# Performance work log

Measured on AMD Instinct MI355X. Metric: run time of the kernel, lower is better.

The kernel has to match this reference:

```python
import jax, jax.numpy as jnp
import numpy as np

N_HEAD = 16

def setup_inputs() -> dict:
    key = jax.random.key(0)
    k1, k2, k3 = jax.random.split(key, 3)
    B, T, C = 4, 2048, 1024
    x = jax.random.normal(k1, (B, T, C), dtype=jnp.float32)
    w_attn = jax.random.normal(k2, (C, 3 * C), dtype=jnp.float32) * 0.02
    w_o = jax.random.normal(k3, (C, C), dtype=jnp.float32) * 0.02
    return {"x": x, "w_attn": w_attn, "w_o": w_o}

def reference(x, w_attn, w_o):
    B, T, C = x.shape
    H = N_HEAD
    hs = C // H
    qkv = x @ w_attn  # [B,T,3C]
    q, k, v = jnp.split(qkv, 3, axis=-1)
    # [B,H,T,hs]
    q = q.reshape(B, T, H, hs).transpose(0, 2, 1, 3)
    k = k.reshape(B, T, H, hs).transpose(0, 2, 1, 3)
    v = v.reshape(B, T, H, hs).transpose(0, 2, 1, 3)
    att = jnp.einsum('bhqd,bhkd->bhqk', q, k) * (1.0 / np.sqrt(hs).astype(np.float32))
    causal = jnp.tril(jnp.ones((T, T), dtype=bool))
    att = jnp.where(causal[None, None], att, jnp.float32(-jnp.inf))
    att = jax.nn.softmax(att, axis=-1)
    y = jnp.einsum('bhqk,bhkd->bhqd', att, v)
    y = y.transpose(0, 2, 1, 3).reshape(B, T, C)
    return y @ w_o
```

## Files before the change

kernel.cpp:

```cpp
#include <hip/hip_runtime.h>

typedef unsigned short u16;
typedef unsigned int u32;
typedef __attribute__((ext_vector_type(8))) __bf16 bf16x8;
typedef __attribute__((ext_vector_type(4))) float f32x4;
typedef __attribute__((ext_vector_type(8))) unsigned short u16x8;
typedef __attribute__((ext_vector_type(4))) unsigned int u32x4;

typedef const __attribute__((address_space(1))) u32 gu32;
typedef __attribute__((address_space(3))) u32 lu32;

__device__ __forceinline__ u16 f2b(float f) {
  u32 u = __builtin_bit_cast(u32, f);
  u32 r = u + 0x7fffu + ((u >> 16) & 1u);
  return (u16)(r >> 16);
}

__device__ __forceinline__ u32 pk2(float lo, float hi) {
  u32 d;
  asm("v_cvt_pk_bf16_f32 %0, %1, %2" : "=v"(d) : "v"(lo), "v"(hi));
  return d;
}

__device__ __forceinline__ bf16x8 pack8(f32x4 a, f32x4 b) {
  u32x4 u;
  u[0] = pk2(a[0], a[1]);
  u[1] = pk2(a[2], a[3]);
  u[2] = pk2(b[0], b[1]);
  u[3] = pk2(b[2], b[3]);
  return __builtin_bit_cast(bf16x8, u);
}

__device__ __forceinline__ bf16x8 ld8(const u16* p) {
  return __builtin_bit_cast(bf16x8, *(const u16x8*)p);
}

__device__ __forceinline__ void gll16(const void* g, void* l) {
  __builtin_amdgcn_global_load_lds((gu32*)g, (lu32*)l, 16, 0, 0);
}

__device__ __forceinline__ f32x4 mfma16(bf16x8 a, bf16x8 b, f32x4 c) {
  return __builtin_amdgcn_mfma_f32_16x16x32_bf16(a, b, c, 0, 0, 0);
}

__global__ void k_cvt(const float* __restrict__ in, u16* __restrict__ out, int n4) {
  int i = blockIdx.x * blockDim.x + threadIdx.x;
  int stride = gridDim.x * blockDim.x;
  for (int idx = i; idx < n4; idx += stride) {
    float4 v = ((const float4*)in)[idx];
    u32 lo = (u32)f2b(v.x) | ((u32)f2b(v.y) << 16);
    u32 hi = (u32)f2b(v.z) | ((u32)f2b(v.w) << 16);
    ((uint2*)out)[idx] = make_uint2(lo, hi);
  }
}

__global__ void k_tr(const float* __restrict__ in, u16* __restrict__ out, int R, int C) {
  __shared__ u16 tile[32][33];
  int bx = blockIdx.x * 32;
  int by = blockIdx.y * 32;
  int tx = threadIdx.x, ty = threadIdx.y;
#pragma unroll
  for (int i = 0; i < 32; i += 8)
    tile[ty + i][tx] = f2b(in[(size_t)(by + ty + i) * C + bx + tx]);
  __syncthreads();
#pragma unroll
  for (int i = 0; i < 32; i += 8)
    out[(size_t)(bx + ty + i) * R + by + tx] = tile[tx][ty + i];
}

template <int EPI>
__global__ __launch_bounds__(256) void k_gemm(const u16* __restrict__ A,
                                              const u16* __restrict__ B,
                                              void* __restrict__ Cp) {
  const int K = 1024;
  __shared__ __align__(16) u16 As[128 * 32];
  __shared__ __align__(16) u16 Bs[128 * 32];
  int tid = threadIdx.x;
  int lane = tid & 63, wid = tid >> 6;
  int wr = wid >> 1, wc = wid & 1;
  int m0 = blockIdx.y * 128, n0 = blockIdx.x * 128;
  int r = lane & 15, qq = lane >> 4;

  const u16* Ag0 = A + (size_t)(m0 + wid * 32 + (lane >> 2)) * K + (lane & 3) * 8;
  const u16* Bg0 = B + (size_t)(n0 + wid * 32 + (lane >> 2)) * K + (lane & 3) * 8;
  u16* Asl0 = As + (wid * 32) * 32;
  u16* Asl1 = As + (wid * 32 + 16) * 32;
  u16* Bsl0 = Bs + (wid * 32) * 32;
  u16* Bsl1 = Bs + (wid * 32 + 16) * 32;

  f32x4 acc[4][4] = {};

  for (int k0 = 0; k0 < K; k0 += 32) {
    gll16(Ag0 + k0, Asl0);
    gll16(Ag0 + 16 * K + k0, Asl1);
    gll16(Bg0 + k0, Bsl0);
    gll16(Bg0 + 16 * K + k0, Bsl1);
    __syncthreads();
    bf16x8 af[4], bfr[4];
#pragma unroll
    for (int m = 0; m < 4; ++m) af[m] = ld8(&As[(wr * 64 + m * 16 + r) * 32 + qq * 8]);
#pragma unroll
    for (int n = 0; n < 4; ++n) bfr[n] = ld8(&Bs[(wc * 64 + n * 16 + r) * 32 + qq * 8]);
#pragma unroll
    for (int m = 0; m < 4; ++m)
#pragma unroll
      for (int n = 0; n < 4; ++n) acc[m][n] = mfma16(af[m], bfr[n], acc[m][n]);
    __syncthreads();
  }

  if constexpr (EPI == 0) {
    u16* qkv = (u16*)Cp;
#pragma unroll
    for (int m = 0; m < 4; ++m) {
      int gr = m0 + wr * 64 + m * 16 + qq * 4;
      int b = gr >> 11, t0 = gr & 2047;
#pragma unroll
      for (int n = 0; n < 4; ++n) {
        int gc = n0 + wc * 64 + n * 16 + r;
        int which = gc >> 10, rem = gc & 1023;
        int hh = rem >> 6, d = rem & 63;
        if (which == 2) {
          u16* dst = qkv + (size_t)2 * 8388608u +
                     ((size_t)((b * 16 + hh) * 64 + d)) * 2048 + t0;
          u32 p0 = pk2(acc[m][n][0], acc[m][n][1]);
          u32 p1 = pk2(acc[m][n][2], acc[m][n][3]);
          *(uint2*)dst = make_uint2(p0, p1);
        } else {
          float sc = (which == 0) ? 0.18033688011112042f : 1.0f;
          u16* dst = qkv + (size_t)which * 8388608u +
                     ((size_t)((b * 16 + hh) * 2048 + t0)) * 64 + d;
#pragma unroll
          for (int i = 0; i < 4; ++i) dst[(size_t)i * 64] = f2b(acc[m][n][i] * sc);
        }
      }
    }
  } else {
    float* out = (float*)Cp;
#pragma unroll
    for (int m = 0; m < 4; ++m) {
      int gr = m0 + wr * 64 + m * 16 + qq * 4;
#pragma unroll
      for (int n = 0; n < 4; ++n) {
        int gc = n0 + wc * 64 + n * 16 + r;
#pragma unroll
        for (int i = 0; i < 4; ++i) out[(size_t)(gr + i) * 1024 + gc] = acc[m][n][i];
      }
    }
  }
}

__global__ __launch_bounds__(256) void k_attn(const u16* __restrict__ Qm,
                                              const u16* __restrict__ Km,
                                              const u16* __restrict__ VTm,
                                              u16* __restrict__ Y) {
  int bi = blockIdx.x;
  int x = bi >> 6;
  int bh = bi & 63;
  int b = bh >> 4, h = bh & 15;
  int qb0 = (15 - x) * 128;
  int tid = threadIdx.x, lane = tid & 63, w = tid >> 6;
  int r = lane & 15, qq = lane >> 4;
  const size_t base = (size_t)bh * (2048 * 64);
  int q0w = qb0 + w * 32;

  __shared__ __align__(16) u16 Kt[2][64 * 64];
  __shared__ __align__(16) u16 Vt[2][64 * 64];

  bf16x8 qf[2][2];
#pragma unroll
  for (int m = 0; m < 2; ++m)
#pragma unroll
    for (int kc = 0; kc < 2; ++kc)
      qf[m][kc] = ld8(Qm + base + (size_t)(q0w + m * 16 + r) * 64 + kc * 32 + qq * 8);

  f32x4 acc[2][4] = {};
  float m_run[2] = {-1e30f, -1e30f};
  float l_run[2] = {0.f, 0.f};
  int ntwg = (qb0 >> 6) + 2;

  int srow = lane >> 3;
  int kch0 = (lane & 7) ^ (srow & 3);
  int kch1 = (lane & 7) ^ ((srow & 3) | 4);
  int vch = (lane & 7) ^ srow;
  const u16* Kg = Km + base;
  const u16* Vg = VTm + base;

  int ar = 8 * (r >> 2) + (r & 3);
  int fkl = (r & 3) | (((r >> 2) & 1) << 2);
  int ks0 = ((qq ^ fkl)) * 8, ks1 = ((qq ^ fkl) ^ 4) * 8;
  int fvl = r & 7;
  int vs0 = ((qq ^ fvl)) * 8, vs1 = ((qq ^ fvl) ^ 4) * 8;

#define STAGE(buf, j0n)                                                                 \
  do {                                                                                  \
    gll16(Kg + (size_t)((j0n) + w * 16 + srow) * 64 + kch0 * 8,                         \
          &Kt[buf][(w * 16) * 64]);                                                     \
    gll16(Kg + (size_t)((j0n) + w * 16 + 8 + srow) * 64 + kch1 * 8,                     \
          &Kt[buf][(w * 16 + 8) * 64]);                                                 \
    gll16(Vg + (size_t)(w * 16 + srow) * 2048 + (j0n) + vch * 8,                        \
          &Vt[buf][(w * 16) * 64]);                                                     \
    gll16(Vg + (size_t)(w * 16 + 8 + srow) * 2048 + (j0n) + vch * 8,                    \
          &Vt[buf][(w * 16 + 8) * 64]);                                                 \
  } while (0)

  STAGE(0, 0);
  __syncthreads();

  for (int it = 0; it < ntwg; ++it) {
    int j0 = it << 6;
    int cur = it & 1;
    bool active = (j0 <= q0w + 31);
    f32x4 s[4][2];
    bf16x8 vfr[4][2];

    if (active) {
      __builtin_amdgcn_s_setprio(1);
#pragma unroll
      for (int nt = 0; nt < 4; ++nt) {
        int knt = 32 * (nt >> 1) + 4 * (nt & 1);
        const u16* kb_ = &Kt[cur][(knt + ar) * 64];
        bf16x8 k0 = ld8(kb_ + ks0);
        bf16x8 k1 = ld8(kb_ + ks1);
#pragma unroll
        for (int m = 0; m < 2; ++m) {
          f32x4 z = {};
          s[nt][m] = mfma16(k1, qf[m][1], mfma16(k0, qf[m][0], z));
        }
      }
#pragma unroll
      for (int n = 0; n < 4; ++n) {
        const u16* vb_ = &Vt[cur][(n * 16 + r) * 64];
        vfr[n][0] = ld8(vb_ + vs0);
        vfr[n][1] = ld8(vb_ + vs1);
      }
      __builtin_amdgcn_s_setprio(0);
    }

    if (it + 1 < ntwg) STAGE(cur ^ 1, j0 + 64);

    if (active) {
      bool nm = (j0 + 63 > q0w);
      if (nm) {
#pragma unroll
        for (int nt = 0; nt < 4; ++nt) {
          int kb = j0 + 32 * (nt >> 1) + 4 * (nt & 1) + 8 * qq;
#pragma unroll
          for (int m = 0; m < 2; ++m) {
            int qg = q0w + m * 16 + r;
#pragma unroll
            for (int i = 0; i < 4; ++i)
              s[nt][m][i] = (kb + i <= qg) ? s[nt][m][i] : -1e30f;
          }
        }
      }

      float tm[2];
#pragma unroll
      for (int m = 0; m < 2; ++m) {
        float t0 = fmaxf(fmaxf(s[0][m][0], s[0][m][1]), fmaxf(s[0][m][2], s[0][m][3]));
        float t1 = fmaxf(fmaxf(s[1][m][0], s[1][m][1]), fmaxf(s[1][m][2], s[1][m][3]));
        float t2 = fmaxf(fmaxf(s[2][m][0], s[2][m][1]), fmaxf(s[2][m][2], s[2][m][3]));
        float t3 = fmaxf(fmaxf(s[3][m][0], s[3][m][1]), fmaxf(s[3][m][2], s[3][m][3]));
        float t = fmaxf(fmaxf(t0, t1), fmaxf(t2, t3));
        t = fmaxf(t, __shfl_xor(t, 16));
        t = fmaxf(t, __shfl_xor(t, 32));
        tm[m] = t;
      }

      int grow = (tm[0] > m_run[0]) | (tm[1] > m_run[1]);
      if (__any(grow)) {
#pragma unroll
        for (int m = 0; m < 2; ++m) {
          float mn = fmaxf(m_run[m], tm[m]);
          float corr = __builtin_amdgcn_exp2f(m_run[m] - mn);
          m_run[m] = mn;
          l_run[m] *= corr;
#pragma unroll
          for (int i = 0; i < 4; ++i) {
            float c = __shfl(corr, qq * 4 + i);
#pragma unroll
            for (int n = 0; n < 4; ++n) acc[m][n][i] *= c;
          }
        }
      }

#pragma unroll
      for (int m = 0; m < 2; ++m) {
        float ls = 0.f;
#pragma unroll
        for (int nt = 0; nt < 4; ++nt)
#pragma unroll
          for (int i = 0; i < 4; ++i) {
            float e = __builtin_amdgcn_exp2f(s[nt][m][i] - m_run[m]);
            s[nt][m][i] = e;
            ls += e;
          }
        l_run[m] += ls;
      }

      __builtin_amdgcn_s_setprio(1);
#pragma unroll
      for (int m = 0; m < 2; ++m) {
        bf16x8 pa0 = pack8(s[0][m], s[1][m]);
        bf16x8 pa1 = pack8(s[2][m], s[3][m]);
#pragma unroll
        for (int n = 0; n < 4; ++n) acc[m][n] = mfma16(pa0, vfr[n][0], acc[m][n]);
#pragma unroll
        for (int n = 0; n < 4; ++n) acc[m][n] = mfma16(pa1, vfr[n][1], acc[m][n]);
      }
      __builtin_amdgcn_s_setprio(0);
    }

    __syncthreads();
  }
#undef STAGE

  float li[2][4];
#pragma unroll
  for (int m = 0; m < 2; ++m) {
    float l = l_run[m];
    l += __shfl_xor(l, 16);
    l += __shfl_xor(l, 32);
    float inv = 1.0f / l;
#pragma unroll
    for (int i = 0; i < 4; ++i) li[m][i] = __shfl(inv, qq * 4 + i);
  }
#pragma unroll
  for (int m = 0; m < 2; ++m)
#pragma unroll
    for (int n = 0; n < 4; ++n)
#pragma unroll
      for (int i = 0; i < 4; ++i)
        Y[((size_t)(b * 2048 + q0w + m * 16 + qq * 4 + i)) * 1024 + h * 64 + n * 16 + r] =
            f2b(acc[m][n][i] * li[m][i]);
}

extern "C" void kernel_launch(void* const* d_in, const int* in_sizes, int n_in,
                              void* d_out, int out_size, void* d_ws, size_t ws_size,
                              hipStream_t stream) {
  const float* x = (const float*)d_in[0];
  const float* w_attn = (const float*)d_in[1];
  const float* w_o = (const float*)d_in[2];
  float* out = (float*)d_out;

  char* ws = (char*)d_ws;
  u16* xb = (u16*)(ws + 0);
  u16* watT = (u16*)(ws + 16777216);
  u16* woT = (u16*)(ws + 23068672);
  u16* qb = (u16*)(ws + 25165824);
  u16* kb = (u16*)(ws + 41943040);
  u16* vb = (u16*)(ws + 58720256);
  u16* yb = (u16*)(ws + 75497472);

  k_cvt<<<2048, 256, 0, stream>>>(x, xb, 8192 * 1024 / 4);
  k_tr<<<dim3(3072 / 32, 1024 / 32), dim3(32, 8), 0, stream>>>(w_attn, watT, 1024, 3072);
  k_tr<<<dim3(1024 / 32, 1024 / 32), dim3(32, 8), 0, stream>>>(w_o, woT, 1024, 1024);
  k_gemm<0><<<dim3(24, 64), 256, 0, stream>>>(xb, watT, (void*)qb);
  k_attn<<<dim3(1024), 256, 0, stream>>>(qb, kb, vb, yb);
  k_gemm<1><<<dim3(8, 64), 256, 0, stream>>>(yb, woT, (void*)out);
}
```

Measured before the change: 205.8 us.

## Double-buffer GEMM LDS tiles with async global-to-LDS prefetch two stages ahead

The GEMM kernel now keeps two LDS buffers for the A and B tiles and issues the global-to-LDS loads for tile k+2 while the MFMAs for tile k run. Explicit vmcnt waits and barriers replace the two __syncthreads per iteration, so the global loads are meant to overlap with compute instead of stalling each K step. This doubles LDS use per block, which may lower occupancy, and it depends on hand-counted vmcnt values being correct.

```diff
diff --git a/kernel.cpp b/kernel.cpp
--- a/kernel.cpp
+++ b/kernel.cpp
@@ -73,8 +73,9 @@
                                               const u16* __restrict__ B,
                                               void* __restrict__ Cp) {
   const int K = 1024;
-  __shared__ __align__(16) u16 As[128 * 32];
-  __shared__ __align__(16) u16 Bs[128 * 32];
+  const int NT = 32;
+  __shared__ __align__(16) u16 As[2][128 * 32];
+  __shared__ __align__(16) u16 Bs[2][128 * 32];
   int tid = threadIdx.x;
   int lane = tid & 63, wid = tid >> 6;
   int wr = wid >> 1, wc = wid & 1;
@@ -83,30 +84,49 @@
 
   const u16* Ag0 = A + (size_t)(m0 + wid * 32 + (lane >> 2)) * K + (lane & 3) * 8;
   const u16* Bg0 = B + (size_t)(n0 + wid * 32 + (lane >> 2)) * K + (lane & 3) * 8;
-  u16* Asl0 = As + (wid * 32) * 32;
-  u16* Asl1 = As + (wid * 32 + 16) * 32;
-  u16* Bsl0 = Bs + (wid * 32) * 32;
-  u16* Bsl1 = Bs + (wid * 32 + 16) * 32;
+  int sl0 = (wid * 32) * 32;
+  int sl1 = (wid * 32 + 16) * 32;
+
+#define GSTAGE(buf, k0)                          \
+  do {                                           \
+    gll16(Ag0 + (k0), &As[buf][sl0]);            \
+    gll16(Ag0 + 16 * K + (k0), &As[buf][sl1]);   \
+    gll16(Bg0 + (k0), &Bs[buf][sl0]);            \
+    gll16(Bg0 + 16 * K + (k0), &Bs[buf][sl1]);   \
+  } while (0)
 
   f32x4 acc[4][4] = {};
 
-  for (int k0 = 0; k0 < K; k0 += 32) {
-    gll16(Ag0 + k0, Asl0);
-    gll16(Ag0 + 16 * K + k0, Asl1);
-    gll16(Bg0 + k0, Bsl0);
-    gll16(Bg0 + 16 * K + k0, Bsl1);
-    __syncthreads();
+  GSTAGE(0, 0);
+  GSTAGE(1, 32);
+
+  for (int kt = 0; kt < NT; ++kt) {
+    int cur = kt & 1;
+    if (kt + 1 < NT)
+      asm volatile("s_waitcnt vmcnt(4)" ::: "memory");
+    else
+      asm volatile("s_waitcnt vmcnt(0)" ::: "memory");
+    __builtin_amdgcn_s_barrier();
+
     bf16x8 af[4], bfr[4];
 #pragma unroll
-    for (int m = 0; m < 4; ++m) af[m] = ld8(&As[(wr * 64 + m * 16 + r) * 32 + qq * 8]);
-#pragma unroll
-    for (int n = 0; n < 4; ++n) bfr[n] = ld8(&Bs[(wc * 64 + n * 16 + r) * 32 + qq * 8]);
-#pragma unroll
     for (int m = 0; m < 4; ++m)
+      af[m] = ld8(&As[cur][(wr * 64 + m * 16 + r) * 32 + qq * 8]);
+#pragma unroll
+    for (int n = 0; n < 4; ++n)
+      bfr[n] = ld8(&Bs[cur][(wc * 64 + n * 16 + r) * 32 + qq * 8]);
+    asm volatile("s_waitcnt lgkmcnt(0)" ::: "memory");
+    __builtin_amdgcn_sched_barrier(0);
+    __builtin_amdgcn_s_barrier();
+
+    if (kt + 2 < NT) GSTAGE(cur, (kt + 2) * 32);
+
+#pragma unroll
+    for (int m = 0; m < 4; ++m)
 #pragma unroll
       for (int n = 0; n < 4; ++n) acc[m][n] = mfma16(af[m], bfr[n], acc[m][n]);
-    __syncthreads();
-  }
+  }
+#undef GSTAGE
 
   if constexpr (EPI == 0) {
     u16* qkv = (u16*)Cp;
```

New measurement: 187.6 us. 1.1x faster.
